# Optimization experiments

Measured on AMD Instinct MI355X. Metric: run time of the kernel, lower is better.

## Reference

```python
import jax, jax.numpy as jnp
import numpy as np

B, N, F_IN = 8, 1024, 64
HEADS = 8
D = F_IN  # out_features per head (in_features == out_features)


def setup_inputs() -> dict:
    key = jax.random.key(0)
    ks = jax.random.split(key, 5)
    stdv = 1.0 / np.sqrt(F_IN * HEADS)
    h = jax.random.normal(ks[0], (B, N, F_IN), dtype=jnp.float32)
    adj = jnp.ones((B, N, N), dtype=jnp.float32)  # passed but unused by the module
    W = jax.random.uniform(ks[1], (F_IN, D * HEADS), minval=-stdv, maxval=stdv, dtype=jnp.float32)
    a = jax.random.uniform(ks[2], (2 * D, 1), minval=-stdv, maxval=stdv, dtype=jnp.float32)
    out_W = jax.random.normal(ks[3], (D * HEADS, F_IN), dtype=jnp.float32) / np.sqrt(D * HEADS)
    out_b = jnp.zeros((F_IN,), dtype=jnp.float32)
    return {"h": h, "adj": adj, "W": W, "a": a, "out_W": out_W, "out_b": out_b}


def reference(h, adj, W, a, out_W, out_b):
    Bv, Nv, _ = h.shape
    Dh = W.shape[1] // HEADS
    # Wh: [B, N, H, D]
    Wh = (h @ W).reshape(Bv, Nv, HEADS, Dh)
    # Additive attention decomposed: e[b,i,j,h] = leaky_relu(Wh[b,i,h].a_src + Wh[b,j,h].a_dst)
    a_src = jnp.einsum('bnhd,d->bnh', Wh, a[:Dh, 0])
    a_dst = jnp.einsum('bnhd,d->bnh', Wh, a[Dh:, 0])
    e = jax.nn.leaky_relu(a_src[:, :, None, :] + a_dst[:, None, :, :], negative_slope=0.01)  # [B,N,N,H]
    # Module applies softmax over dim=1 (the first node axis i)
    attn = jax.nn.softmax(e, axis=1)  # [B,N,N,H]
    # h_prime[b,i,h,:] = sum_j attn[b,i,j,h] * Wh[b,j,h,:]
    h_prime = jnp.einsum('bijh,bjhd->bihd', attn, Wh).reshape(Bv, Nv, HEADS * Dh)
    return h_prime @ out_W + out_b
```

## Files before the change

### kernel.cpp

```cpp
#include <hip/hip_runtime.h>


#define B_  8
#define N_  1024
#define H_  8
#define D_  64
#define BH_ 64
#define CH_ 32
#define CL_ 32

__device__ __forceinline__ float bcast_lane(float v, int l) {
  return __int_as_float(__builtin_amdgcn_readlane(__float_as_int(v), l));
}

__global__ __launch_bounds__(256) void k_wh(
    const float* __restrict__ h, const float* __restrict__ W,
    const float* __restrict__ a,
    float* __restrict__ Wh, float* __restrict__ sArr, float* __restrict__ tArr) {
  const int tid = threadIdx.x;
  const int lane = tid & 63;
  const int wid = tid >> 6;
  const int row0 = blockIdx.x * 16;
  const int b = row0 >> 10;

  float hreg[16];
#pragma unroll
  for (int r = 0; r < 16; ++r) hreg[r] = h[(row0 + r) * 64 + lane];
  const float a_s = a[lane];
  const float a_t = a[64 + lane];

  float acc0[16], acc1[16];
#pragma unroll
  for (int r = 0; r < 16; ++r) { acc0[r] = 0.f; acc1[r] = 0.f; }
#pragma unroll 4
  for (int k = 0; k < 64; ++k) {
    const float w0 = W[k * 512 + tid];
    const float w1 = W[k * 512 + tid + 256];
#pragma unroll
    for (int r = 0; r < 16; ++r) {
      const float hv = bcast_lane(hreg[r], k);
      acc0[r] += hv * w0;
      acc1[r] += hv * w1;
    }
  }
  const int hh0 = wid, hh1 = wid + 4;
#pragma unroll
  for (int r = 0; r < 16; ++r) {
    const int n = (row0 + r) & (N_ - 1);
    Wh[((b * H_ + hh0) * N_ + n) * D_ + lane] = acc0[r];
    Wh[((b * H_ + hh1) * N_ + n) * D_ + lane] = acc1[r];
  }
#pragma unroll
  for (int r = 0; r < 16; ++r) {
    const int n = (row0 + r) & (N_ - 1);
    float s0 = acc0[r] * a_s, t0 = acc0[r] * a_t;
    float s1 = acc1[r] * a_s, t1 = acc1[r] * a_t;
#pragma unroll
    for (int m = 32; m > 0; m >>= 1) {
      s0 += __shfl_xor(s0, m); t0 += __shfl_xor(t0, m);
      s1 += __shfl_xor(s1, m); t1 += __shfl_xor(t1, m);
    }
    if (lane == 0) {
      sArr[(b * H_ + hh0) * N_ + n] = s0;
      tArr[(b * H_ + hh0) * N_ + n] = t0;
      sArr[(b * H_ + hh1) * N_ + n] = s1;
      tArr[(b * H_ + hh1) * N_ + n] = t1;
    }
  }
}

__global__ __launch_bounds__(1024) void k_sort(
    const float* __restrict__ sArr, const float* __restrict__ tArr,
    const float* __restrict__ Wh,
    int* __restrict__ tsi, float2* __restrict__ uvArr,
    int* __restrict__ qrk, float2* __restrict__ cOff) {
  __shared__ float sL[1024];
  __shared__ float tvL[1024];
  __shared__ int   tiL[1024];
  __shared__ float cum1L[1024], cum001L[1024];
  __shared__ float2 wsT[16 * 64];
  __shared__ float ws1[16], ws2[16];
  const int tid = threadIdx.x;
  const int lane = tid & 63;
  const int wv_ = tid >> 6;
  const int bh = blockIdx.x;

  const float orig_s = sArr[bh * N_ + tid];
  float sv_r = orig_s;
  float tv_r = tArr[bh * N_ + tid];
  int   ti_r = tid;

  for (int size = 2; size <= 1024; size <<= 1) {
    for (int stride = size >> 1; stride > 0; stride >>= 1) {
      const bool up = ((tid & size) == 0);
      const bool lower = ((tid & stride) == 0);
      float psv, ptv; int pti;
      if (stride >= 64) {
        sL[tid] = sv_r; tvL[tid] = tv_r; tiL[tid] = ti_r;
        __syncthreads();
        const int p = tid ^ stride;
        psv = sL[p]; ptv = tvL[p]; pti = tiL[p];
        __syncthreads();
      } else {
        psv = __shfl_xor(sv_r, stride);
        ptv = __shfl_xor(tv_r, stride);
        pti = __shfl_xor(ti_r, stride);
      }
      const bool sameDir = (up == lower);
      const bool pLessS = (psv < sv_r);
      if (pLessS == sameDir) sv_r = psv;
      const bool pLessT = (ptv < tv_r) || (ptv == tv_r && pti < ti_r);
      if (pLessT == sameDir) { tv_r = ptv; ti_r = pti; }
    }
  }
  sL[tid] = sv_r; tvL[tid] = tv_r;

  float c1 = __expf(sv_r), c001 = __expf(0.01f * sv_r);
  {
    float a1 = c1, a2 = c001;
#pragma unroll
    for (int off = 1; off < 64; off <<= 1) {
      const float x1 = __shfl_up(a1, off);
      const float x2 = __shfl_up(a2, off);
      if (lane >= off) { a1 += x1; a2 += x2; }
    }
    if (lane == 63) { ws1[wv_] = a1; ws2[wv_] = a2; }
    __syncthreads();
    float o1 = 0.f, o2 = 0.f;
    for (int ww = 0; ww < 16; ++ww) {
      if (ww < wv_) { o1 += ws1[ww]; o2 += ws2[ww]; }
    }
    c1 = a1 + o1; c001 = a2 + o2;
  }
  cum1L[tid] = c1; cum001L[tid] = c001;
  __syncthreads();
  const float totalHi = cum1L[1023];

  float u_r, v_r;
  {
    const float tj = tv_r;
    const float th = -tj;
    int lo = 0, hi = 1024;
    while (lo < hi) { const int mid = (lo + hi) >> 1; if (sL[mid] <= th) lo = mid + 1; else hi = mid; }
    const float S_lo = (lo > 0) ? cum001L[lo - 1] : 0.f;
    const float S_hi = totalHi - ((lo > 0) ? cum1L[lo - 1] : 0.f);
    const float et = __expf(tj), et001 = __expf(0.01f * tj);
    const float Z = et * S_hi + et001 * S_lo;
    u_r = et / Z; v_r = et001 / Z;
    uvArr[bh * N_ + tid] = make_float2(u_r, v_r);
    tsi[bh * N_ + tid] = ti_r;
  }
  {
    const float th = -orig_s;
    int lo = 0, hi = 1024;
    while (lo < hi) { const int mid = (lo + hi) >> 1; if (tvL[mid] <= th) lo = mid + 1; else hi = mid; }
    qrk[bh * N_ + tid] = lo;
  }

  const int whb = bh * (N_ * D_);
  float r1a = 0.f, r2a = 0.f, r1b = 0.f, r2b = 0.f;
#pragma unroll 8
  for (int k2 = 0; k2 < CL_; ++k2) {
    const int   ja = __builtin_amdgcn_readlane(ti_r, k2);
    const float ua = bcast_lane(u_r, k2);
    const float va = bcast_lane(v_r, k2);
    const int   jb = __builtin_amdgcn_readlane(ti_r, 32 + k2);
    const float ub = bcast_lane(u_r, 32 + k2);
    const float vb = bcast_lane(v_r, 32 + k2);
    const float wa = Wh[whb + ja * 64 + lane];
    const float wb = Wh[whb + jb * 64 + lane];
    r1a += ua * wa; r2a += va * wa;
    r1b += ub * wb; r2b += vb * wb;
  }
  wsT[wv_ * 64 + lane] = make_float2(r1a + r1b, r2a + r2b);
  __syncthreads();
  float o1 = 0.f, o2 = 0.f;
  for (int ww = 0; ww < 16; ++ww) {
    if (ww < wv_) { const float2 t = wsT[ww * 64 + lane]; o1 += t.x; o2 += t.y; }
  }
  const int cb = bh * 33;
  cOff[(cb + 2 * wv_) * 64 + lane]     = make_float2(o1, o2);
  cOff[(cb + 2 * wv_ + 1) * 64 + lane] = make_float2(o1 + r1a, o2 + r2a);
  if (wv_ == 15)
    cOff[(cb + 32) * 64 + lane] = make_float2(o1 + r1a + r1b, o2 + r2a + r2b);
}

__global__ __launch_bounds__(64) void k_inc(
    const float* __restrict__ Wh, const int* __restrict__ tsi,
    const float2* __restrict__ uvArr, const float2* __restrict__ cOff,
    float2* __restrict__ INC12) {
  const int blk = blockIdx.x;
  const int bh = ((blk >> 8) << 3) | (blk & 7);
  const int c  = (blk >> 3) & 31;
  const int d = threadIdx.x;
  const float2 off = cOff[(bh * 33 + c) * 64 + d];
  float r1 = off.x, r2 = off.y;
  const int base = bh * N_ + c * CL_;
  const int whb = bh * (N_ * D_);
#pragma unroll 8
  for (int k2 = 0; k2 < CL_; ++k2) {
    const int j = tsi[base + k2];
    const float2 uv = uvArr[base + k2];
    const float w = Wh[whb + j * 64 + d];
    r1 += uv.x * w;
    r2 += uv.y * w;
    INC12[(base + k2) * 64 + d] = make_float2(r1, r2);
  }
}

__global__ __launch_bounds__(512) void k_out(
    const float* __restrict__ sArr, const int* __restrict__ qrk,
    const float2* __restrict__ INC12, const float2* __restrict__ cOff,
    const float* __restrict__ outW, const float* __restrict__ outb,
    float* __restrict__ out) {
  __shared__ float part[8 * 8 * 64];
  __shared__ int   rkI[16 * 8];
  __shared__ float esL[16 * 8], es001L[16 * 8];
  const int tid = threadIdx.x;
  const int row0 = blockIdx.x * 16;
  const int b = row0 >> 10;
  const int p = tid >> 6;
  const int lane = tid & 63;

  if (tid < 128) {
    const int r = tid >> 3, hh = tid & 7;
    const int bh = b * H_ + hh;
    const int n = (row0 + r) & (N_ - 1);
    const float si = sArr[bh * N_ + n];
    rkI[tid] = qrk[bh * N_ + n];
    esL[tid] = __expf(si);
    es001L[tid] = __expf(0.01f * si);
  }
  __syncthreads();

  float hpv[16];
  {
    const int bh = b * H_ + p;
    const float T1 = cOff[(bh * 33 + 32) * 64 + lane].x;
#pragma unroll
    for (int r = 0; r < 16; ++r) {
      const int rk = rkI[r * 8 + p];
      float i1 = 0.f, i2 = 0.f;
      if (rk > 0) {
        const float2 I = INC12[(bh * N_ + rk - 1) * 64 + lane];
        i1 = I.x; i2 = I.y;
      }
      hpv[r] = esL[r * 8 + p] * (T1 - i1) + es001L[r * 8 + p] * i2;
    }
  }

  float acc[16];
#pragma unroll
  for (int r = 0; r < 16; ++r) acc[r] = 0.f;
#pragma unroll 4
  for (int kc = 0; kc < 64; ++kc) {
    const float wvv = outW[(p * 64 + kc) * 64 + lane];
#pragma unroll
    for (int r = 0; r < 16; ++r) {
      const float hv = bcast_lane(hpv[r], kc);
      acc[r] += hv * wvv;
    }
  }

  for (int half = 0; half < 2; ++half) {
#pragma unroll
    for (int r = 0; r < 8; ++r) part[(p * 8 + r) * 64 + lane] = acc[half * 8 + r];
    __syncthreads();
    {
      const int r2 = tid >> 6, c2 = tid & 63;
      float ssum = 0.f;
#pragma unroll
      for (int p2 = 0; p2 < 8; ++p2) ssum += part[(p2 * 8 + r2) * 64 + c2];
      out[(row0 + half * 8 + r2) * 64 + c2] = outb[c2] + ssum;
    }
    __syncthreads();
  }
}

extern "C" void kernel_launch(void* const* d_in, const int* in_sizes, int n_in,
                              void* d_out, int out_size, void* d_ws, size_t ws_size,
                              hipStream_t stream) {
  const float* h    = (const float*)d_in[0];
  const float* W    = (const float*)d_in[2];
  const float* a    = (const float*)d_in[3];
  const float* outW = (const float*)d_in[4];
  const float* outb = (const float*)d_in[5];
  float* out = (float*)d_out;

  float* ws   = (float*)d_ws;
  float* Wh   = ws;
  float* sArr = Wh + (size_t)BH_ * N_ * D_;
  float* tArr = sArr + BH_ * N_;
  int*   tsi  = (int*)(tArr + BH_ * N_);
  int*   qrk  = tsi + BH_ * N_;
  float2* uvArr = (float2*)(qrk + BH_ * N_);
  float2* cOff  = uvArr + (size_t)BH_ * N_;
  float2* INC12 = cOff + (size_t)BH_ * 33 * 64;

  hipLaunchKernelGGL(k_wh,   dim3((B_ * N_) / 16), dim3(256), 0, stream,
                     h, W, a, Wh, sArr, tArr);
  hipLaunchKernelGGL(k_sort, dim3(BH_), dim3(1024), 0, stream,
                     sArr, tArr, Wh, tsi, uvArr, qrk, cOff);
  hipLaunchKernelGGL(k_inc,  dim3(BH_ * CH_), dim3(64), 0, stream,
                     Wh, tsi, uvArr, cOff, INC12);
  hipLaunchKernelGGL(k_out,  dim3((B_ * N_) / 16), dim3(512), 0, stream,
                     sArr, qrk, INC12, cOff, outW, outb, out);
}
```

Before: 158.8 us.

## Fuse sort and incremental prefix kernels, replicating sort across four blocks per head

Merges the k_inc pass into the sort kernel. The sorted indices and u/v weights now stay in shared memory instead of going through global tsi/uvArr arrays, and one kernel launch is removed. To keep the GPU busy, each (batch, head) is handled by four blocks; each block redoes the full bitonic sort, scans and chunk offsets and then computes the INC12 prefix for its 8 chunks. Each block also writes only its quarter of the qrk ranks, and cOff is written by only one block per head. The cost is four times the redundant sort and scan work, plus larger shared-memory use per block.

Result: no change. 156.0 us (-1.8%).

```diff
diff --git a/kernel.cpp b/kernel.cpp
--- a/kernel.cpp
+++ b/kernel.cpp
@@ -69,21 +69,23 @@
   }
 }
 
-__global__ __launch_bounds__(1024) void k_sort(
+__global__ __launch_bounds__(1024) void k_sortinc(
     const float* __restrict__ sArr, const float* __restrict__ tArr,
     const float* __restrict__ Wh,
-    int* __restrict__ tsi, float2* __restrict__ uvArr,
-    int* __restrict__ qrk, float2* __restrict__ cOff) {
+    int* __restrict__ qrk, float2* __restrict__ cOff,
+    float2* __restrict__ INC12) {
   __shared__ float sL[1024];
   __shared__ float tvL[1024];
   __shared__ int   tiL[1024];
   __shared__ float cum1L[1024], cum001L[1024];
   __shared__ float2 wsT[16 * 64];
+  __shared__ float2 chOff[CH_ * 64];
   __shared__ float ws1[16], ws2[16];
   const int tid = threadIdx.x;
   const int lane = tid & 63;
   const int wv_ = tid >> 6;
-  const int bh = blockIdx.x;
+  const int bi = blockIdx.x;
+  const int bh = bi & 63, q = bi >> 6;
 
   const float orig_s = sArr[bh * N_ + tid];
   float sv_r = orig_s;
@@ -113,7 +115,7 @@
       if (pLessT == sameDir) { tv_r = ptv; ti_r = pti; }
     }
   }
-  sL[tid] = sv_r; tvL[tid] = tv_r;
+  sL[tid] = sv_r; tvL[tid] = tv_r; tiL[tid] = ti_r;
 
   float c1 = __expf(sv_r), c001 = __expf(0.01f * sv_r);
   {
@@ -147,15 +149,15 @@
     const float et = __expf(tj), et001 = __expf(0.01f * tj);
     const float Z = et * S_hi + et001 * S_lo;
     u_r = et / Z; v_r = et001 / Z;
-    uvArr[bh * N_ + tid] = make_float2(u_r, v_r);
-    tsi[bh * N_ + tid] = ti_r;
-  }
-  {
+  }
+  if ((tid >> 8) == q) {
     const float th = -orig_s;
     int lo = 0, hi = 1024;
     while (lo < hi) { const int mid = (lo + hi) >> 1; if (tvL[mid] <= th) lo = mid + 1; else hi = mid; }
     qrk[bh * N_ + tid] = lo;
   }
+  __syncthreads();
+  cum1L[tid] = u_r; cum001L[tid] = v_r;
 
   const int whb = bh * (N_ * D_);
   float r1a = 0.f, r2a = 0.f, r1b = 0.f, r2b = 0.f;
@@ -178,33 +180,32 @@
   for (int ww = 0; ww < 16; ++ww) {
     if (ww < wv_) { const float2 t = wsT[ww * 64 + lane]; o1 += t.x; o2 += t.y; }
   }
-  const int cb = bh * 33;
-  cOff[(cb + 2 * wv_) * 64 + lane]     = make_float2(o1, o2);
-  cOff[(cb + 2 * wv_ + 1) * 64 + lane] = make_float2(o1 + r1a, o2 + r2a);
-  if (wv_ == 15)
-    cOff[(cb + 32) * 64 + lane] = make_float2(o1 + r1a + r1b, o2 + r2a + r2b);
-}
-
-__global__ __launch_bounds__(64) void k_inc(
-    const float* __restrict__ Wh, const int* __restrict__ tsi,
-    const float2* __restrict__ uvArr, const float2* __restrict__ cOff,
-    float2* __restrict__ INC12) {
-  const int blk = blockIdx.x;
-  const int bh = ((blk >> 8) << 3) | (blk & 7);
-  const int c  = (blk >> 3) & 31;
-  const int d = threadIdx.x;
-  const float2 off = cOff[(bh * 33 + c) * 64 + d];
-  float r1 = off.x, r2 = off.y;
-  const int base = bh * N_ + c * CL_;
-  const int whb = bh * (N_ * D_);
+  chOff[(2 * wv_) * 64 + lane]     = make_float2(o1, o2);
+  chOff[(2 * wv_ + 1) * 64 + lane] = make_float2(o1 + r1a, o2 + r2a);
+  if (q == 0) {
+    const int cb = bh * 33;
+    cOff[(cb + 2 * wv_) * 64 + lane]     = make_float2(o1, o2);
+    cOff[(cb + 2 * wv_ + 1) * 64 + lane] = make_float2(o1 + r1a, o2 + r2a);
+    if (wv_ == 15)
+      cOff[(cb + 32) * 64 + lane] = make_float2(o1 + r1a + r1b, o2 + r2a + r2b);
+  }
+  __syncthreads();
+
+  if (wv_ < 8) {
+    const int cc = q * 8 + wv_;
+    const float2 off = chOff[cc * 64 + lane];
+    float r1 = off.x, r2 = off.y;
+    const int rb = bh * N_ + cc * CL_;
 #pragma unroll 8
-  for (int k2 = 0; k2 < CL_; ++k2) {
-    const int j = tsi[base + k2];
-    const float2 uv = uvArr[base + k2];
-    const float w = Wh[whb + j * 64 + d];
-    r1 += uv.x * w;
-    r2 += uv.y * w;
-    INC12[(base + k2) * 64 + d] = make_float2(r1, r2);
+    for (int k2 = 0; k2 < CL_; ++k2) {
+      const int   j  = tiL[cc * CL_ + k2];
+      const float uu = cum1L[cc * CL_ + k2];
+      const float vv = cum001L[cc * CL_ + k2];
+      const float w  = Wh[whb + j * 64 + lane];
+      r1 += uu * w;
+      r2 += vv * w;
+      INC12[(rb + k2) * 64 + lane] = make_float2(r1, r2);
+    }
   }
 }
 
@@ -291,18 +292,14 @@
   float* Wh   = ws;
   float* sArr = Wh + (size_t)BH_ * N_ * D_;
   float* tArr = sArr + BH_ * N_;
-  int*   tsi  = (int*)(tArr + BH_ * N_);
-  int*   qrk  = tsi + BH_ * N_;
-  float2* uvArr = (float2*)(qrk + BH_ * N_);
-  float2* cOff  = uvArr + (size_t)BH_ * N_;
+  int*   qrk  = (int*)(tArr + BH_ * N_);
+  float2* cOff  = (float2*)(qrk + BH_ * N_);
   float2* INC12 = cOff + (size_t)BH_ * 33 * 64;
 
-  hipLaunchKernelGGL(k_wh,   dim3((B_ * N_) / 16), dim3(256), 0, stream,
+  hipLaunchKernelGGL(k_wh,      dim3((B_ * N_) / 16), dim3(256), 0, stream,
                      h, W, a, Wh, sArr, tArr);
-  hipLaunchKernelGGL(k_sort, dim3(BH_), dim3(1024), 0, stream,
-                     sArr, tArr, Wh, tsi, uvArr, qrk, cOff);
-  hipLaunchKernelGGL(k_inc,  dim3(BH_ * CH_), dim3(64), 0, stream,
-                     Wh, tsi, uvArr, cOff, INC12);
-  hipLaunchKernelGGL(k_out,  dim3((B_ * N_) / 16), dim3(512), 0, stream,
+  hipLaunchKernelGGL(k_sortinc, dim3(256), dim3(1024), 0, stream,
+                     sArr, tArr, Wh, qrk, cOff, INC12);
+  hipLaunchKernelGGL(k_out,     dim3((B_ * N_) / 16), dim3(512), 0, stream,
                      sArr, qrk, INC12, cOff, outW, outb, out);
 }
```
